# Kernel optimization log

Measured on AMD Instinct MI355X. Metric: run time of the kernel, lower is better.

## Reference

```python
import jax, jax.numpy as jnp
import numpy as np

HEADS = 8
GROUP_SIZE = 256
DIM = 512
QK_DIM = 512
M_GLOBAL = 64


def setup_inputs() -> dict:
    key = jax.random.key(0)
    ks = jax.random.split(key, 9)
    B, N = 2, 16384
    normed_x = jax.random.normal(ks[0], (B, N, DIM), dtype=jnp.float32)
    # idx_last must be a per-batch permutation of [0, N): gather reorders tokens,
    # the final scatter puts them back.
    perm = jnp.stack([jax.random.permutation(jax.random.fold_in(ks[1], b), N) for b in range(B)])
    idx_last = perm[..., None].astype(jnp.int32)  # [B, N, 1]
    dq = QK_DIM // HEADS
    dv = DIM // HEADS
    k_global = jax.random.normal(ks[2], (HEADS, M_GLOBAL, dq), dtype=jnp.float32)
    v_global = jax.random.normal(ks[3], (HEADS, M_GLOBAL, dv), dtype=jnp.float32)
    s = 0.02
    Wq = jax.random.normal(ks[4], (DIM, QK_DIM), dtype=jnp.float32) * s
    Wk = jax.random.normal(ks[5], (DIM, QK_DIM), dtype=jnp.float32) * s
    Wv = jax.random.normal(ks[6], (DIM, DIM), dtype=jnp.float32) * s
    Wproj = jax.random.normal(ks[7], (DIM, DIM), dtype=jnp.float32) * s
    return {"normed_x": normed_x, "idx_last": idx_last, "k_global": k_global,
            "v_global": v_global, "Wq": Wq, "Wk": Wk, "Wv": Wv, "Wproj": Wproj}


def _iasa_forward(normed_x, idx_last, k_global, v_global, Wq, Wk, Wv, Wproj):
    B, N, dim = normed_x.shape
    H = HEADS
    gs = min(N, GROUP_SIZE)
    ng = -(-N // gs)
    pad_n = ng * gs - N
    q = normed_x @ Wq  # [B, N, qk]
    k = normed_x @ Wk  # [B, N, qk]
    v = normed_x @ Wv  # [B, N, dim]
    # gather-reorder tokens
    q = jnp.take_along_axis(q, jnp.broadcast_to(idx_last, q.shape), axis=1)
    k = jnp.take_along_axis(k, jnp.broadcast_to(idx_last, k.shape), axis=1)
    v = jnp.take_along_axis(v, jnp.broadcast_to(idx_last, v.shape), axis=1)
    # pad queries with flipped tail to [B, ng*gs, qk]
    pq = jnp.concatenate([q, q[:, N - pad_n:N][:, ::-1]], axis=1)
    # pad k/v with flipped last (pad_n+gs) tokens -> length (ng+1)*gs
    pk = jnp.concatenate([k, k[:, N - pad_n - gs:N][:, ::-1]], axis=1)
    pv = jnp.concatenate([v, v[:, N - pad_n - gs:N][:, ::-1]], axis=1)
    dq = pq.shape[-1] // H
    dv = dim // H
    # queries: [B, ng, H, gs, dq]
    qg = pq.reshape(B, ng, gs, H, dq).transpose(0, 1, 3, 2, 4)
    # overlapping windows of size 2*gs, stride gs (unfold equivalent)
    kgrp = pk.reshape(B, ng + 1, gs, H, dq)
    vgrp = pv.reshape(B, ng + 1, gs, H, dv)
    kwin = jnp.concatenate([kgrp[:, :-1], kgrp[:, 1:]], axis=2).transpose(0, 1, 3, 2, 4)  # [B,ng,H,2gs,dq]
    vwin = jnp.concatenate([vgrp[:, :-1], vgrp[:, 1:]], axis=2).transpose(0, 1, 3, 2, 4)  # [B,ng,H,2gs,dv]
    scale = 1.0 / jnp.sqrt(jnp.asarray(dq, dtype=qg.dtype))
    # local attention
    s1 = jnp.einsum('bghqd,bghkd->bghqk', qg, kwin) * scale
    out1 = jnp.einsum('bghqk,bghkd->bghqd', jax.nn.softmax(s1, axis=-1), vwin)
    # global attention (k_global/v_global shared across batch and groups)
    s2 = jnp.einsum('bghqd,hmd->bghqm', qg, k_global) * scale
    out2 = jnp.einsum('bghqm,hmd->bghqd', jax.nn.softmax(s2, axis=-1), v_global)
    out = (out1 + out2).transpose(0, 1, 3, 2, 4).reshape(B, ng * gs, H * dv)[:, :N]
    # scatter back (inverse of the gather, since idx_last is a permutation)
    idxo = jnp.broadcast_to(idx_last, out.shape)
    bi = jnp.arange(B)[:, None, None]
    ci = jnp.arange(H * dv)[None, None, :]
    out = out.at[bi, idxo, ci].set(out)
    return out @ Wproj


def reference(normed_x, idx_last, k_global, v_global, Wq, Wk, Wv, Wproj):
    return _iasa_forward(normed_x, idx_last, k_global, v_global, Wq, Wk, Wv, Wproj)
```

## Files before the change

### kernel.cpp

```cpp
#include <hip/hip_runtime.h>
#include <hip/hip_bf16.h>

#define B_   2
#define N_   16384
#define H_   8
#define GS_  256
#define NG_  64

typedef unsigned short u16;
typedef __attribute__((ext_vector_type(8))) short bf16x8;
typedef __attribute__((ext_vector_type(4))) float f32x4;
typedef __attribute__((ext_vector_type(8))) unsigned short us8;
typedef __attribute__((ext_vector_type(4))) unsigned short us4;
typedef __attribute__((ext_vector_type(4))) unsigned int u32x4;

__device__ __forceinline__ u16 f2b(float f){
  union { float f; unsigned u; } v; v.f = f;
  unsigned r = v.u + 0x7fffu + ((v.u >> 16) & 1u);
  return (u16)(r >> 16);
}

__device__ __forceinline__ u16 f2bh(float f){
  __hip_bfloat16 h = __float2bfloat16(f);
  u16 u; __builtin_memcpy(&u, &h, 2);
  return u;
}

__device__ __forceinline__ void gload16(const void* g, const void* lds){
  __builtin_amdgcn_global_load_lds(
      (const __attribute__((address_space(1))) void*)g,
      (__attribute__((address_space(3))) void*)lds, 16, 0, 0);
}

__device__ __forceinline__ bf16x8 lds_read8(const u16* base, int row, int coloff){
  int byte = (row*128 + coloff) ^ ((row & 7) << 4);
  return *(const bf16x8*)((const char*)base + byte);
}

__device__ __forceinline__ void stout(float* p, float v){ *p = v; }
__device__ __forceinline__ void stout(u16* p, float v){ *p = f2b(v); }

__global__ void cvt_f32_bf16(const float4* __restrict__ in, us4* __restrict__ out, int n4){
  int i = blockIdx.x * 256 + threadIdx.x;
  if (i < n4){
    float4 v = in[i];
    us4 o;
    o[0] = f2b(v.x); o[1] = f2b(v.y); o[2] = f2b(v.z); o[3] = f2b(v.w);
    out[i] = o;
  }
}

__global__ void cvt_w_t(const float* __restrict__ W0, const float* __restrict__ W1,
                        const float* __restrict__ W2, const float* __restrict__ W3,
                        u16* __restrict__ T0, u16* __restrict__ T1,
                        u16* __restrict__ T2, u16* __restrict__ T3)
{
  int z = blockIdx.z;
  const float* W = (z==0)?W0:((z==1)?W1:((z==2)?W2:W3));
  u16* T = (z==0)?T0:((z==1)?T1:((z==2)?T2:T3));
  __shared__ float tile[16][17];
  int tx = threadIdx.x & 15, ty = threadIdx.x >> 4;
  int k0 = blockIdx.x*16, n0 = blockIdx.y*16;
  tile[ty][tx] = W[(k0+ty)*512 + n0 + tx];
  __syncthreads();
  T[(n0+ty)*512 + k0 + tx] = f2b(tile[tx][ty]);
}

template<typename OUT_T, bool MULTI, bool GATHA, bool SCATC>
__global__ __launch_bounds__(256, 2) void gemm_bf16k(
    const u16* __restrict__ A,
    const u16* __restrict__ Wt0, const u16* __restrict__ Wt1, const u16* __restrict__ Wt2,
    const int* __restrict__ perm,
    OUT_T* __restrict__ C, int ldc)
{
  __shared__ u16 Al[128*64];
  __shared__ u16 Bl[128*64];
  const int tid = threadIdx.x;
  const int l = tid & 63, w = tid >> 6;
  const int lr = l & 15, lg = l >> 4;
  const int bm = blockIdx.x, bn = blockIdx.y;
  const int wr = (w >> 1) * 64, wc = (w & 1) * 64;

  const u16* Wt; int ocolb; float qsc;
  if (MULTI){
    int wsel = bn >> 2;
    Wt = (wsel == 0) ? Wt0 : ((wsel == 1) ? Wt1 : Wt2);
    ocolb = (bn & 3) * 128;
    qsc = (wsel == 0) ? 0.125f : 1.0f;
  } else { Wt = Wt0; ocolb = bn * 128; qsc = 1.0f; }

  int arows[4];
#pragma unroll
  for (int i = 0; i < 4; ++i){
    int r = bm*128 + i*32 + (tid >> 3);
    arows[i] = GATHA ? ((r & ~(N_-1)) + perm[r]) : r;
  }

  f32x4 acc[4][4];
#pragma unroll
  for (int m = 0; m < 4; ++m)
#pragma unroll
    for (int n = 0; n < 4; ++n) acc[m][n] = (f32x4){0.f,0.f,0.f,0.f};

  const int c8 = tid & 7;
  for (int kk = 0; kk < 512; kk += 64){
#pragma unroll
    for (int i = 0; i < 4; ++i){
      int o = i*4096 + tid*16;
      int brow = o >> 7;
      gload16(A  + (size_t)arows[i]*512 + kk + c8*8, (const char*)Al + i*4096 + w*1024);
      gload16(Wt + (size_t)(ocolb + brow)*512 + kk + c8*8, (const char*)Bl + i*4096 + w*1024);
    }
    __syncthreads();
#pragma unroll
    for (int ks = 0; ks < 2; ++ks){
      bf16x8 af[4], bfv[4];
#pragma unroll
      for (int m = 0; m < 4; ++m) af[m]  = *(const bf16x8*)&Al[(wr + m*16 + lr)*64 + ks*32 + lg*8];
#pragma unroll
      for (int n = 0; n < 4; ++n) bfv[n] = *(const bf16x8*)&Bl[(wc + n*16 + lr)*64 + ks*32 + lg*8];
#pragma unroll
      for (int m = 0; m < 4; ++m)
#pragma unroll
        for (int n = 0; n < 4; ++n)
          acc[m][n] = __builtin_amdgcn_mfma_f32_16x16x32_bf16(af[m], bfv[n], acc[m][n], 0, 0, 0);
    }
    __syncthreads();
  }
#pragma unroll
  for (int m = 0; m < 4; ++m)
#pragma unroll
    for (int n = 0; n < 4; ++n)
#pragma unroll
      for (int j = 0; j < 4; ++j){
        int row = bm*128 + wr + m*16 + lg*4 + j;
        int col = bn*128 + wc + n*16 + lr;
        size_t orow = SCATC ? (size_t)((row & ~(N_-1)) + perm[row]) : (size_t)row;
        stout(&C[orow*ldc + col], acc[m][n][j] * qsc);
      }
}

#define COMPUTE_CHUNK(KBUF, VBUF, ACC, LAC) do { \
  f32x4 s_[4][4]; \
  _Pragma("unroll") \
  for (int m_ = 0; m_ < 4; ++m_){ _Pragma("unroll") for (int n_ = 0; n_ < 4; ++n_) s_[m_][n_] = (f32x4){0.f,0.f,0.f,0.f}; } \
  _Pragma("unroll") \
  for (int ks_ = 0; ks_ < 2; ++ks_){ \
    bf16x8 kf_[4]; \
    _Pragma("unroll") for (int n_ = 0; n_ < 4; ++n_) kf_[n_] = lds_read8((KBUF), n_*16 + lr, ks_*64 + lg*16); \
    _Pragma("unroll") for (int m_ = 0; m_ < 4; ++m_){ \
      _Pragma("unroll") for (int n_ = 0; n_ < 4; ++n_) \
        s_[m_][n_] = __builtin_amdgcn_mfma_f32_16x16x32_bf16(qf[m_][ks_], kf_[n_], s_[m_][n_], 0, 0, 0); } } \
  _Pragma("unroll") \
  for (int m_ = 0; m_ < 4; ++m_){ _Pragma("unroll") for (int j_ = 0; j_ < 4; ++j_){ \
      float rs_ = 0.f; \
      _Pragma("unroll") for (int n_ = 0; n_ < 4; ++n_){ float p_ = __expf(s_[m_][n_][j_]); s_[m_][n_][j_] = p_; rs_ += p_; } \
      (LAC)[m_][j_] += rs_; } } \
  _Pragma("unroll") \
  for (int mh_ = 0; mh_ < 2; ++mh_){ \
    _Pragma("unroll") for (int m2_ = 0; m2_ < 2; ++m2_){ \
      _Pragma("unroll") for (int n_ = 0; n_ < 4; ++n_){ \
        _Pragma("unroll") for (int j_ = 0; j_ < 4; ++j_){ \
          int row_ = m2_*16 + lg*4 + j_, col_ = n_*16 + lr; \
          int byte_ = (row_*128 + col_*2) ^ ((row_ & 7) << 4); \
          *(u16*)((char*)Pw + byte_) = f2bh(s_[mh_*2+m2_][n_][j_]); } } } \
    _Pragma("unroll") for (int ks_ = 0; ks_ < 2; ++ks_){ \
      bf16x8 pa_[2], vb_[4]; \
      _Pragma("unroll") for (int m2_ = 0; m2_ < 2; ++m2_) pa_[m2_] = lds_read8(Pw, m2_*16 + lr, ks_*64 + lg*16); \
      _Pragma("unroll") for (int n_ = 0; n_ < 4; ++n_) vb_[n_] = lds_read8((VBUF), n_*16 + lr, ks_*64 + lg*16); \
      _Pragma("unroll") for (int m2_ = 0; m2_ < 2; ++m2_){ \
        _Pragma("unroll") for (int n_ = 0; n_ < 4; ++n_) \
          (ACC)[mh_*2+m2_][n_] = __builtin_amdgcn_mfma_f32_16x16x32_bf16(pa_[m2_], vb_[n_], (ACC)[mh_*2+m2_][n_], 0, 0, 0); } } \
  } \
} while(0)

#define LOADKV(c) do { int c_ = (c); \
  if (c_ < 8){ \
    int p0k_ = g*GS_ + c_*64 + krow_; \
    int p1k_ = p0k_ + 32; \
    int rk0_ = (p0k_ < N_) ? p0k_ : (2*N_ - 1 - p0k_); \
    int rk1_ = (p1k_ < N_) ? p1k_ : (2*N_ - 1 - p1k_); \
    kr0 = *(const us8*)(qkv + (size_t)(b*N_ + rk0_)*1536 + 512 + h*64 + kc8_*8); \
    kr1 = *(const us8*)(qkv + (size_t)(b*N_ + rk1_)*1536 + 512 + h*64 + kc8_*8); \
    int p0v_ = g*GS_ + c_*64 + 2*pair; \
    int p1v_ = p0v_ + 1; \
    int rv0_ = (p0v_ < N_) ? p0v_ : (2*N_ - 1 - p0v_); \
    int rv1_ = (p1v_ < N_) ? p1v_ : (2*N_ - 1 - p1v_); \
    vr0 = *(const us8*)(qkv + (size_t)(b*N_ + rv0_)*1536 + 1024 + h*64 + dvb*8); \
    vr1 = *(const us8*)(qkv + (size_t)(b*N_ + rv1_)*1536 + 1024 + h*64 + dvb*8); \
  } else { \
    kr0 = *(const us8*)(kgb + (size_t)(h*64 + krow_)*64 + kc8_*8); \
    kr1 = *(const us8*)(kgb + (size_t)(h*64 + 32 + krow_)*64 + kc8_*8); \
    vr0 = *(const us8*)(vgb + (size_t)(h*64 + 2*pair)*64 + dvb*8); \
    vr1 = *(const us8*)(vgb + (size_t)(h*64 + 2*pair + 1)*64 + dvb*8); \
  } } while(0)

#define WRITEKV() do { \
  { int r0_ = krow_, r1_ = 32 + krow_; \
    *(us8*)((char*)Kb + ((r0_*128 + kc8_*16) ^ ((r0_ & 7) << 4))) = kr0; \
    *(us8*)((char*)Kb + ((r1_*128 + kc8_*16) ^ ((r1_ & 7) << 4))) = kr1; } \
  _Pragma("unroll") \
  for (int j_ = 0; j_ < 8; ++j_){ \
    int r_ = dvb*8 + j_; \
    int byte_ = (r_*128 + pair*4) ^ ((r_ & 7) << 4); \
    *(unsigned*)((char*)Vb + byte_) = (unsigned)vr0[j_] | ((unsigned)vr1[j_] << 16); } \
} while(0)

__global__ __launch_bounds__(256, 2) void attn_kernel(
    const u16* __restrict__ qkv,
    const u16* __restrict__ kgb,
    const u16* __restrict__ vgb,
    u16* __restrict__ outp)
{
  __shared__ u16 Pl[4][32*64];
  __shared__ u16 Kb[64*64];
  __shared__ u16 Vb[64*64];

  const int tid = threadIdx.x;
  const int l = tid & 63, w = tid >> 6;
  const int lr = l & 15, lg = l >> 4;
  const int pair = tid & 31, dvb = tid >> 5;
  const int krow_ = tid >> 3, kc8_ = tid & 7;

  const int g = blockIdx.x, h = blockIdx.y, b = blockIdx.z;

  bf16x8 qf[4][2];
#pragma unroll
  for (int m = 0; m < 4; ++m){
    int grow = g*GS_ + w*64 + m*16 + lr;
    const u16* qrow = qkv + (size_t)(b*N_ + grow)*1536 + h*64;
#pragma unroll
    for (int ks = 0; ks < 2; ++ks)
      qf[m][ks] = *(const bf16x8*)(qrow + ks*32 + lg*8);
  }

  u16* Pw = Pl[w];

  us8 kr0, kr1, vr0, vr1;
  LOADKV(0);
  WRITEKV();
  __syncthreads();

  f32x4 oacc[4][4];
  float lrun[4][4];
#pragma unroll
  for (int m = 0; m < 4; ++m)
#pragma unroll
    for (int n = 0; n < 4; ++n) oacc[m][n] = (f32x4){0.f,0.f,0.f,0.f};
#pragma unroll
  for (int m = 0; m < 4; ++m)
#pragma unroll
    for (int j = 0; j < 4; ++j) lrun[m][j] = 0.f;

  for (int c = 0; c < 8; ++c){
    LOADKV(c + 1);
    COMPUTE_CHUNK(Kb, Vb, oacc, lrun);
    __syncthreads();
    WRITEKV();
    __syncthreads();
  }

#pragma unroll
  for (int m = 0; m < 4; ++m)
#pragma unroll
    for (int j = 0; j < 4; ++j){
      float s1 = lrun[m][j];
      s1 += __shfl_xor(s1, 1); s1 += __shfl_xor(s1, 2);
      s1 += __shfl_xor(s1, 4); s1 += __shfl_xor(s1, 8);
      float i1 = 1.f / s1;
#pragma unroll
      for (int n = 0; n < 4; ++n) oacc[m][n][j] *= i1;
    }

  {
    f32x4 s_[4][4];
#pragma unroll
    for (int m_ = 0; m_ < 4; ++m_)
#pragma unroll
      for (int n_ = 0; n_ < 4; ++n_) s_[m_][n_] = (f32x4){0.f,0.f,0.f,0.f};
#pragma unroll
    for (int ks_ = 0; ks_ < 2; ++ks_){
      bf16x8 kf_[4];
#pragma unroll
      for (int n_ = 0; n_ < 4; ++n_) kf_[n_] = lds_read8(Kb, n_*16 + lr, ks_*64 + lg*16);
#pragma unroll
      for (int m_ = 0; m_ < 4; ++m_)
#pragma unroll
        for (int n_ = 0; n_ < 4; ++n_)
          s_[m_][n_] = __builtin_amdgcn_mfma_f32_16x16x32_bf16(qf[m_][ks_], kf_[n_], s_[m_][n_], 0, 0, 0);
    }
#pragma unroll
    for (int m_ = 0; m_ < 4; ++m_)
#pragma unroll
      for (int j_ = 0; j_ < 4; ++j_){
        float rs_ = 0.f;
#pragma unroll
        for (int n_ = 0; n_ < 4; ++n_){ float p_ = __expf(s_[m_][n_][j_]); s_[m_][n_][j_] = p_; rs_ += p_; }
        rs_ += __shfl_xor(rs_, 1); rs_ += __shfl_xor(rs_, 2);
        rs_ += __shfl_xor(rs_, 4); rs_ += __shfl_xor(rs_, 8);
        float iv_ = 1.f / rs_;
#pragma unroll
        for (int n_ = 0; n_ < 4; ++n_) s_[m_][n_][j_] *= iv_;
      }
#pragma unroll
    for (int mh_ = 0; mh_ < 2; ++mh_){
#pragma unroll
      for (int m2_ = 0; m2_ < 2; ++m2_){
#pragma unroll
        for (int n_ = 0; n_ < 4; ++n_){
#pragma unroll
          for (int j_ = 0; j_ < 4; ++j_){
            int row_ = m2_*16 + lg*4 + j_, col_ = n_*16 + lr;
            int byte_ = (row_*128 + col_*2) ^ ((row_ & 7) << 4);
            *(u16*)((char*)Pw + byte_) = f2bh(s_[mh_*2+m2_][n_][j_]);
          }
        }
      }
#pragma unroll
      for (int ks_ = 0; ks_ < 2; ++ks_){
        bf16x8 pa_[2], vb_[4];
#pragma unroll
        for (int m2_ = 0; m2_ < 2; ++m2_) pa_[m2_] = lds_read8(Pw, m2_*16 + lr, ks_*64 + lg*16);
#pragma unroll
        for (int n_ = 0; n_ < 4; ++n_) vb_[n_] = lds_read8(Vb, n_*16 + lr, ks_*64 + lg*16);
#pragma unroll
        for (int m2_ = 0; m2_ < 2; ++m2_)
#pragma unroll
          for (int n_ = 0; n_ < 4; ++n_)
            oacc[mh_*2+m2_][n_] = __builtin_amdgcn_mfma_f32_16x16x32_bf16(pa_[m2_], vb_[n_], oacc[mh_*2+m2_][n_], 0, 0, 0);
      }
    }
  }

#pragma unroll
  for (int mh = 0; mh < 2; ++mh){
#pragma unroll
    for (int m2 = 0; m2 < 2; ++m2)
#pragma unroll
      for (int n = 0; n < 4; ++n)
#pragma unroll
        for (int j = 0; j < 4; ++j){
          int row = m2*16 + lg*4 + j, col = n*16 + lr;
          int byte = (row*128 + col*2) ^ ((row & 7) << 4);
          *(u16*)((char*)Pw + byte) = f2bh(oacc[mh*2+m2][n][j]);
        }
    __builtin_amdgcn_s_waitcnt(0);
#pragma unroll
    for (int i4 = 0; i4 < 4; ++i4){
      int o = i4*1024 + l*16;
      int row = o >> 7, c8 = (o & 127) >> 4;
      int addr = o ^ ((row & 7) << 4);
      u32x4 d = *(const u32x4*)((const char*)Pw + addr);
      int orow = g*GS_ + w*64 + mh*32 + row;
      *(u32x4*)(outp + (size_t)(b*N_ + orow)*512 + h*64 + c8*8) = d;
    }
  }
}

extern "C" void kernel_launch(void* const* d_in, const int* in_sizes, int n_in,
                              void* d_out, int out_size, void* d_ws, size_t ws_size,
                              hipStream_t stream)
{
  const float* x  = (const float*)d_in[0];
  const int*  idx = (const int*)d_in[1];
  const float* kg = (const float*)d_in[2];
  const float* vg = (const float*)d_in[3];
  const float* Wq = (const float*)d_in[4];
  const float* Wk = (const float*)d_in[5];
  const float* Wv = (const float*)d_in[6];
  const float* Wp = (const float*)d_in[7];
  float* out = (float*)d_out;

  char* ws = (char*)d_ws;
  u16* Xb   = (u16*)ws;
  u16* qkv  = (u16*)(ws + 33554432);
  u16* Wqt  = (u16*)(ws + 134217728);
  u16* Wkt  = (u16*)(ws + 134217728 + 524288);
  u16* Wvt  = (u16*)(ws + 134217728 + 2*524288);
  u16* Wpt  = (u16*)(ws + 134217728 + 3*524288);
  u16* kgb  = (u16*)(ws + 134217728 + 4*524288);
  u16* vgb  = (u16*)(ws + 134217728 + 4*524288 + 65536);
  u16* attn_o = Xb;

  cvt_f32_bf16<<<16384, 256, 0, stream>>>((const float4*)x, (us4*)Xb, 16777216/4);
  cvt_f32_bf16<<<32, 256, 0, stream>>>((const float4*)kg, (us4*)kgb, 32768/4);
  cvt_f32_bf16<<<32, 256, 0, stream>>>((const float4*)vg, (us4*)vgb, 32768/4);
  cvt_w_t<<<dim3(32,32,4), 256, 0, stream>>>(Wq, Wk, Wv, Wp, Wqt, Wkt, Wvt, Wpt);
  gemm_bf16k<u16, true, true, false><<<dim3(256,12), 256, 0, stream>>>(Xb, Wqt, Wkt, Wvt, idx, qkv, 1536);
  attn_kernel<<<dim3(64,8,2), 256, 0, stream>>>(qkv, kgb, vgb, attn_o);
  gemm_bf16k<float, false, false, true><<<dim3(256,4), 256, 0, stream>>>(attn_o, Wpt, Wpt, Wpt, idx, out, 512);
}
```

Before: 220.5 us.

## Split attention blocks to 128 queries and use exp2 with log2e-folded scale

```diff
diff --git a/kernel.cpp b/kernel.cpp
--- a/kernel.cpp
+++ b/kernel.cpp
@@ -86,7 +86,7 @@
     int wsel = bn >> 2;
     Wt = (wsel == 0) ? Wt0 : ((wsel == 1) ? Wt1 : Wt2);
     ocolb = (bn & 3) * 128;
-    qsc = (wsel == 0) ? 0.125f : 1.0f;
+    qsc = (wsel == 0) ? 0.18033688f : 1.0f;
   } else { Wt = Wt0; ocolb = bn * 128; qsc = 1.0f; }
 
   int arows[4];
@@ -141,37 +141,35 @@
 }
 
 #define COMPUTE_CHUNK(KBUF, VBUF, ACC, LAC) do { \
-  f32x4 s_[4][4]; \
-  _Pragma("unroll") \
-  for (int m_ = 0; m_ < 4; ++m_){ _Pragma("unroll") for (int n_ = 0; n_ < 4; ++n_) s_[m_][n_] = (f32x4){0.f,0.f,0.f,0.f}; } \
+  f32x4 s_[2][4]; \
+  _Pragma("unroll") \
+  for (int m_ = 0; m_ < 2; ++m_){ _Pragma("unroll") for (int n_ = 0; n_ < 4; ++n_) s_[m_][n_] = (f32x4){0.f,0.f,0.f,0.f}; } \
   _Pragma("unroll") \
   for (int ks_ = 0; ks_ < 2; ++ks_){ \
     bf16x8 kf_[4]; \
     _Pragma("unroll") for (int n_ = 0; n_ < 4; ++n_) kf_[n_] = lds_read8((KBUF), n_*16 + lr, ks_*64 + lg*16); \
-    _Pragma("unroll") for (int m_ = 0; m_ < 4; ++m_){ \
+    _Pragma("unroll") for (int m_ = 0; m_ < 2; ++m_){ \
       _Pragma("unroll") for (int n_ = 0; n_ < 4; ++n_) \
         s_[m_][n_] = __builtin_amdgcn_mfma_f32_16x16x32_bf16(qf[m_][ks_], kf_[n_], s_[m_][n_], 0, 0, 0); } } \
   _Pragma("unroll") \
-  for (int m_ = 0; m_ < 4; ++m_){ _Pragma("unroll") for (int j_ = 0; j_ < 4; ++j_){ \
+  for (int m_ = 0; m_ < 2; ++m_){ _Pragma("unroll") for (int j_ = 0; j_ < 4; ++j_){ \
       float rs_ = 0.f; \
-      _Pragma("unroll") for (int n_ = 0; n_ < 4; ++n_){ float p_ = __expf(s_[m_][n_][j_]); s_[m_][n_][j_] = p_; rs_ += p_; } \
+      _Pragma("unroll") for (int n_ = 0; n_ < 4; ++n_){ float p_ = exp2f(s_[m_][n_][j_]); s_[m_][n_][j_] = p_; rs_ += p_; } \
       (LAC)[m_][j_] += rs_; } } \
   _Pragma("unroll") \
-  for (int mh_ = 0; mh_ < 2; ++mh_){ \
-    _Pragma("unroll") for (int m2_ = 0; m2_ < 2; ++m2_){ \
-      _Pragma("unroll") for (int n_ = 0; n_ < 4; ++n_){ \
-        _Pragma("unroll") for (int j_ = 0; j_ < 4; ++j_){ \
-          int row_ = m2_*16 + lg*4 + j_, col_ = n_*16 + lr; \
-          int byte_ = (row_*128 + col_*2) ^ ((row_ & 7) << 4); \
-          *(u16*)((char*)Pw + byte_) = f2bh(s_[mh_*2+m2_][n_][j_]); } } } \
-    _Pragma("unroll") for (int ks_ = 0; ks_ < 2; ++ks_){ \
-      bf16x8 pa_[2], vb_[4]; \
-      _Pragma("unroll") for (int m2_ = 0; m2_ < 2; ++m2_) pa_[m2_] = lds_read8(Pw, m2_*16 + lr, ks_*64 + lg*16); \
-      _Pragma("unroll") for (int n_ = 0; n_ < 4; ++n_) vb_[n_] = lds_read8((VBUF), n_*16 + lr, ks_*64 + lg*16); \
-      _Pragma("unroll") for (int m2_ = 0; m2_ < 2; ++m2_){ \
-        _Pragma("unroll") for (int n_ = 0; n_ < 4; ++n_) \
-          (ACC)[mh_*2+m2_][n_] = __builtin_amdgcn_mfma_f32_16x16x32_bf16(pa_[m2_], vb_[n_], (ACC)[mh_*2+m2_][n_], 0, 0, 0); } } \
-  } \
+  for (int m_ = 0; m_ < 2; ++m_){ _Pragma("unroll") for (int n_ = 0; n_ < 4; ++n_){ \
+      _Pragma("unroll") for (int j_ = 0; j_ < 4; ++j_){ \
+        int row_ = m_*16 + lg*4 + j_, col_ = n_*16 + lr; \
+        int byte_ = (row_*128 + col_*2) ^ ((row_ & 7) << 4); \
+        *(u16*)((char*)Pw + byte_) = f2bh(s_[m_][n_][j_]); } } } \
+  _Pragma("unroll") \
+  for (int ks_ = 0; ks_ < 2; ++ks_){ \
+    bf16x8 pa_[2], vb_[4]; \
+    _Pragma("unroll") for (int m_ = 0; m_ < 2; ++m_) pa_[m_] = lds_read8(Pw, m_*16 + lr, ks_*64 + lg*16); \
+    _Pragma("unroll") for (int n_ = 0; n_ < 4; ++n_) vb_[n_] = lds_read8((VBUF), n_*16 + lr, ks_*64 + lg*16); \
+    _Pragma("unroll") for (int m_ = 0; m_ < 2; ++m_){ \
+      _Pragma("unroll") for (int n_ = 0; n_ < 4; ++n_) \
+        (ACC)[m_][n_] = __builtin_amdgcn_mfma_f32_16x16x32_bf16(pa_[m_], vb_[n_], (ACC)[m_][n_], 0, 0, 0); } } \
 } while(0)
 
 #define LOADKV(c) do { int c_ = (c); \
@@ -222,12 +220,14 @@
   const int pair = tid & 31, dvb = tid >> 5;
   const int krow_ = tid >> 3, kc8_ = tid & 7;
 
-  const int g = blockIdx.x, h = blockIdx.y, b = blockIdx.z;
-
-  bf16x8 qf[4][2];
-#pragma unroll
-  for (int m = 0; m < 4; ++m){
-    int grow = g*GS_ + w*64 + m*16 + lr;
+  const int g2 = blockIdx.x, h = blockIdx.y, b = blockIdx.z;
+  const int g = g2 >> 1;
+  const int qbase = g2*128 + w*32;
+
+  bf16x8 qf[2][2];
+#pragma unroll
+  for (int m = 0; m < 2; ++m){
+    int grow = qbase + m*16 + lr;
     const u16* qrow = qkv + (size_t)(b*N_ + grow)*1536 + h*64;
 #pragma unroll
     for (int ks = 0; ks < 2; ++ks)
@@ -241,14 +241,14 @@
   WRITEKV();
   __syncthreads();
 
-  f32x4 oacc[4][4];
-  float lrun[4][4];
-#pragma unroll
-  for (int m = 0; m < 4; ++m)
+  f32x4 oacc[2][4];
+  float lrun[2][4];
+#pragma unroll
+  for (int m = 0; m < 2; ++m)
 #pragma unroll
     for (int n = 0; n < 4; ++n) oacc[m][n] = (f32x4){0.f,0.f,0.f,0.f};
 #pragma unroll
-  for (int m = 0; m < 4; ++m)
+  for (int m = 0; m < 2; ++m)
 #pragma unroll
     for (int j = 0; j < 4; ++j) lrun[m][j] = 0.f;
 
@@ -261,7 +261,7 @@
   }
 
 #pragma unroll
-  for (int m = 0; m < 4; ++m)
+  for (int m = 0; m < 2; ++m)
 #pragma unroll
     for (int j = 0; j < 4; ++j){
       float s1 = lrun[m][j];
@@ -273,9 +273,9 @@
     }
 
   {
-    f32x4 s_[4][4];
-#pragma unroll
-    for (int m_ = 0; m_ < 4; ++m_)
+    f32x4 s_[2][4];
+#pragma unroll
+    for (int m_ = 0; m_ < 2; ++m_)
 #pragma unroll
       for (int n_ = 0; n_ < 4; ++n_) s_[m_][n_] = (f32x4){0.f,0.f,0.f,0.f};
 #pragma unroll
@@ -284,18 +284,18 @@
 #pragma unroll
       for (int n_ = 0; n_ < 4; ++n_) kf_[n_] = lds_read8(Kb, n_*16 + lr, ks_*64 + lg*16);
 #pragma unroll
-      for (int m_ = 0; m_ < 4; ++m_)
+      for (int m_ = 0; m_ < 2; ++m_)
 #pragma unroll
         for (int n_ = 0; n_ < 4; ++n_)
           s_[m_][n_] = __builtin_amdgcn_mfma_f32_16x16x32_bf16(qf[m_][ks_], kf_[n_], s_[m_][n_], 0, 0, 0);
     }
 #pragma unroll
-    for (int m_ = 0; m_ < 4; ++m_)
+    for (int m_ = 0; m_ < 2; ++m_)
 #pragma unroll
       for (int j_ = 0; j_ < 4; ++j_){
         float rs_ = 0.f;
 #pragma unroll
-        for (int n_ = 0; n_ < 4; ++n_){ float p_ = __expf(s_[m_][n_][j_]); s_[m_][n_][j_] = p_; rs_ += p_; }
+        for (int n_ = 0; n_ < 4; ++n_){ float p_ = exp2f(s_[m_][n_][j_]); s_[m_][n_][j_] = p_; rs_ += p_; }
         rs_ += __shfl_xor(rs_, 1); rs_ += __shfl_xor(rs_, 2);
         rs_ += __shfl_xor(rs_, 4); rs_ += __shfl_xor(rs_, 8);
         float iv_ = 1.f / rs_;
@@ -303,57 +303,49 @@
         for (int n_ = 0; n_ < 4; ++n_) s_[m_][n_][j_] *= iv_;
       }
 #pragma unroll
-    for (int mh_ = 0; mh_ < 2; ++mh_){
-#pragma unroll
-      for (int m2_ = 0; m2_ < 2; ++m2_){
-#pragma unroll
-        for (int n_ = 0; n_ < 4; ++n_){
-#pragma unroll
-          for (int j_ = 0; j_ < 4; ++j_){
-            int row_ = m2_*16 + lg*4 + j_, col_ = n_*16 + lr;
-            int byte_ = (row_*128 + col_*2) ^ ((row_ & 7) << 4);
-            *(u16*)((char*)Pw + byte_) = f2bh(s_[mh_*2+m2_][n_][j_]);
-          }
+    for (int m_ = 0; m_ < 2; ++m_)
+#pragma unroll
+      for (int n_ = 0; n_ < 4; ++n_)
+#pragma unroll
+        for (int j_ = 0; j_ < 4; ++j_){
+          int row_ = m_*16 + lg*4 + j_, col_ = n_*16 + lr;
+          int byte_ = (row_*128 + col_*2) ^ ((row_ & 7) << 4);
+          *(u16*)((char*)Pw + byte_) = f2bh(s_[m_][n_][j_]);
         }
+#pragma unroll
+    for (int ks_ = 0; ks_ < 2; ++ks_){
+      bf16x8 pa_[2], vb_[4];
+#pragma unroll
+      for (int m_ = 0; m_ < 2; ++m_) pa_[m_] = lds_read8(Pw, m_*16 + lr, ks_*64 + lg*16);
+#pragma unroll
+      for (int n_ = 0; n_ < 4; ++n_) vb_[n_] = lds_read8(Vb, n_*16 + lr, ks_*64 + lg*16);
+#pragma unroll
+      for (int m_ = 0; m_ < 2; ++m_)
+#pragma unroll
+        for (int n_ = 0; n_ < 4; ++n_)
+          oacc[m_][n_] = __builtin_amdgcn_mfma_f32_16x16x32_bf16(pa_[m_], vb_[n_], oacc[m_][n_], 0, 0, 0);
+    }
+  }
+
+#pragma unroll
+  for (int m = 0; m < 2; ++m)
+#pragma unroll
+    for (int n = 0; n < 4; ++n)
+#pragma unroll
+      for (int j = 0; j < 4; ++j){
+        int row = m*16 + lg*4 + j, col = n*16 + lr;
+        int byte = (row*128 + col*2) ^ ((row & 7) << 4);
+        *(u16*)((char*)Pw + byte) = f2bh(oacc[m][n][j]);
       }
-#pragma unroll
-      for (int ks_ = 0; ks_ < 2; ++ks_){
-        bf16x8 pa_[2], vb_[4];
-#pragma unroll
-        for (int m2_ = 0; m2_ < 2; ++m2_) pa_[m2_] = lds_read8(Pw, m2_*16 + lr, ks_*64 + lg*16);
-#pragma unroll
-        for (int n_ = 0; n_ < 4; ++n_) vb_[n_] = lds_read8(Vb, n_*16 + lr, ks_*64 + lg*16);
-#pragma unroll
-        for (int m2_ = 0; m2_ < 2; ++m2_)
-#pragma unroll
-          for (int n_ = 0; n_ < 4; ++n_)
-            oacc[mh_*2+m2_][n_] = __builtin_amdgcn_mfma_f32_16x16x32_bf16(pa_[m2_], vb_[n_], oacc[mh_*2+m2_][n_], 0, 0, 0);
-      }
-    }
-  }
-
-#pragma unroll
-  for (int mh = 0; mh < 2; ++mh){
-#pragma unroll
-    for (int m2 = 0; m2 < 2; ++m2)
-#pragma unroll
-      for (int n = 0; n < 4; ++n)
-#pragma unroll
-        for (int j = 0; j < 4; ++j){
-          int row = m2*16 + lg*4 + j, col = n*16 + lr;
-          int byte = (row*128 + col*2) ^ ((row & 7) << 4);
-          *(u16*)((char*)Pw + byte) = f2bh(oacc[mh*2+m2][n][j]);
-        }
-    __builtin_amdgcn_s_waitcnt(0);
-#pragma unroll
-    for (int i4 = 0; i4 < 4; ++i4){
-      int o = i4*1024 + l*16;
-      int row = o >> 7, c8 = (o & 127) >> 4;
-      int addr = o ^ ((row & 7) << 4);
-      u32x4 d = *(const u32x4*)((const char*)Pw + addr);
-      int orow = g*GS_ + w*64 + mh*32 + row;
-      *(u32x4*)(outp + (size_t)(b*N_ + orow)*512 + h*64 + c8*8) = d;
-    }
+  __builtin_amdgcn_s_waitcnt(0);
+#pragma unroll
+  for (int i4 = 0; i4 < 4; ++i4){
+    int o = i4*1024 + l*16;
+    int row = o >> 7, c8 = (o & 127) >> 4;
+    int addr = o ^ ((row & 7) << 4);
+    u32x4 d = *(const u32x4*)((const char*)Pw + addr);
+    int orow = qbase + row;
+    *(u32x4*)(outp + (size_t)(b*N_ + orow)*512 + h*64 + c8*8) = d;
   }
 }
 
@@ -387,6 +379,6 @@
   cvt_f32_bf16<<<32, 256, 0, stream>>>((const float4*)vg, (us4*)vgb, 32768/4);
   cvt_w_t<<<dim3(32,32,4), 256, 0, stream>>>(Wq, Wk, Wv, Wp, Wqt, Wkt, Wvt, Wpt);
   gemm_bf16k<u16, true, true, false><<<dim3(256,12), 256, 0, stream>>>(Xb, Wqt, Wkt, Wvt, idx, qkv, 1536);
-  attn_kernel<<<dim3(64,8,2), 256, 0, stream>>>(qkv, kgb, vgb, attn_o);
+  attn_kernel<<<dim3(128,8,2), 256, 0, stream>>>(qkv, kgb, vgb, attn_o);
   gemm_bf16k<float, false, false, true><<<dim3(256,4), 256, 0, stream>>>(attn_o, Wpt, Wpt, Wpt, idx, out, 512);
 }
```

After: 225.2 us. +2.1%, slower.

## Compute transposed scores so P tiles pack into vector LDS stores, use exp2

Applied to the files above, without the earlier changes.

```diff
diff --git a/kernel.cpp b/kernel.cpp
--- a/kernel.cpp
+++ b/kernel.cpp
@@ -13,6 +13,7 @@
 typedef __attribute__((ext_vector_type(8))) unsigned short us8;
 typedef __attribute__((ext_vector_type(4))) unsigned short us4;
 typedef __attribute__((ext_vector_type(4))) unsigned int u32x4;
+typedef __attribute__((ext_vector_type(2))) unsigned int u32x2;
 
 __device__ __forceinline__ u16 f2b(float f){
   union { float f; unsigned u; } v; v.f = f;
@@ -24,6 +25,10 @@
   __hip_bfloat16 h = __float2bfloat16(f);
   u16 u; __builtin_memcpy(&u, &h, 2);
   return u;
+}
+
+__device__ __forceinline__ unsigned pk2(float a, float b){
+  return ((unsigned)f2b(b) << 16) | (unsigned)f2b(a);
 }
 
 __device__ __forceinline__ void gload16(const void* g, const void* lds){
@@ -86,7 +91,7 @@
     int wsel = bn >> 2;
     Wt = (wsel == 0) ? Wt0 : ((wsel == 1) ? Wt1 : Wt2);
     ocolb = (bn & 3) * 128;
-    qsc = (wsel == 0) ? 0.125f : 1.0f;
+    qsc = (wsel == 0) ? 0.18033688f : 1.0f;
   } else { Wt = Wt0; ocolb = bn * 128; qsc = 1.0f; }
 
   int arows[4];
@@ -143,27 +148,32 @@
 #define COMPUTE_CHUNK(KBUF, VBUF, ACC, LAC) do { \
   f32x4 s_[4][4]; \
   _Pragma("unroll") \
-  for (int m_ = 0; m_ < 4; ++m_){ _Pragma("unroll") for (int n_ = 0; n_ < 4; ++n_) s_[m_][n_] = (f32x4){0.f,0.f,0.f,0.f}; } \
+  for (int n_ = 0; n_ < 4; ++n_){ _Pragma("unroll") for (int m_ = 0; m_ < 4; ++m_) s_[n_][m_] = (f32x4){0.f,0.f,0.f,0.f}; } \
   _Pragma("unroll") \
   for (int ks_ = 0; ks_ < 2; ++ks_){ \
     bf16x8 kf_[4]; \
     _Pragma("unroll") for (int n_ = 0; n_ < 4; ++n_) kf_[n_] = lds_read8((KBUF), n_*16 + lr, ks_*64 + lg*16); \
-    _Pragma("unroll") for (int m_ = 0; m_ < 4; ++m_){ \
-      _Pragma("unroll") for (int n_ = 0; n_ < 4; ++n_) \
-        s_[m_][n_] = __builtin_amdgcn_mfma_f32_16x16x32_bf16(qf[m_][ks_], kf_[n_], s_[m_][n_], 0, 0, 0); } } \
+    _Pragma("unroll") for (int n_ = 0; n_ < 4; ++n_){ \
+      _Pragma("unroll") for (int m_ = 0; m_ < 4; ++m_) \
+        s_[n_][m_] = __builtin_amdgcn_mfma_f32_16x16x32_bf16(kf_[n_], qf[m_][ks_], s_[n_][m_], 0, 0, 0); } } \
   _Pragma("unroll") \
-  for (int m_ = 0; m_ < 4; ++m_){ _Pragma("unroll") for (int j_ = 0; j_ < 4; ++j_){ \
-      float rs_ = 0.f; \
-      _Pragma("unroll") for (int n_ = 0; n_ < 4; ++n_){ float p_ = __expf(s_[m_][n_][j_]); s_[m_][n_][j_] = p_; rs_ += p_; } \
-      (LAC)[m_][j_] += rs_; } } \
+  for (int m_ = 0; m_ < 4; ++m_){ \
+    float rs_ = 0.f; \
+    _Pragma("unroll") for (int n_ = 0; n_ < 4; ++n_){ \
+      _Pragma("unroll") for (int j_ = 0; j_ < 4; ++j_){ \
+        float p_ = exp2f(s_[n_][m_][j_]); s_[n_][m_][j_] = p_; rs_ += p_; } } \
+    (LAC)[m_] += rs_; } \
   _Pragma("unroll") \
   for (int mh_ = 0; mh_ < 2; ++mh_){ \
     _Pragma("unroll") for (int m2_ = 0; m2_ < 2; ++m2_){ \
+      int m_ = mh_*2 + m2_; \
+      int q_ = m2_*16 + lr; \
       _Pragma("unroll") for (int n_ = 0; n_ < 4; ++n_){ \
-        _Pragma("unroll") for (int j_ = 0; j_ < 4; ++j_){ \
-          int row_ = m2_*16 + lg*4 + j_, col_ = n_*16 + lr; \
-          int byte_ = (row_*128 + col_*2) ^ ((row_ & 7) << 4); \
-          *(u16*)((char*)Pw + byte_) = f2bh(s_[mh_*2+m2_][n_][j_]); } } } \
+        u32x2 pk_; \
+        pk_[0] = pk2(s_[n_][m_][0], s_[n_][m_][1]); \
+        pk_[1] = pk2(s_[n_][m_][2], s_[n_][m_][3]); \
+        int byte_ = (q_*128 + n_*32 + lg*8) ^ ((q_ & 7) << 4); \
+        *(u32x2*)((char*)Pw + byte_) = pk_; } } \
     _Pragma("unroll") for (int ks_ = 0; ks_ < 2; ++ks_){ \
       bf16x8 pa_[2], vb_[4]; \
       _Pragma("unroll") for (int m2_ = 0; m2_ < 2; ++m2_) pa_[m2_] = lds_read8(Pw, m2_*16 + lr, ks_*64 + lg*16); \
@@ -242,15 +252,13 @@
   __syncthreads();
 
   f32x4 oacc[4][4];
-  float lrun[4][4];
+  float lrun[4];
 #pragma unroll
   for (int m = 0; m < 4; ++m)
 #pragma unroll
     for (int n = 0; n < 4; ++n) oacc[m][n] = (f32x4){0.f,0.f,0.f,0.f};
 #pragma unroll
-  for (int m = 0; m < 4; ++m)
-#pragma unroll
-    for (int j = 0; j < 4; ++j) lrun[m][j] = 0.f;
+  for (int m = 0; m < 4; ++m) lrun[m] = 0.f;
 
   for (int c = 0; c < 8; ++c){
     LOADKV(c + 1);
@@ -260,60 +268,68 @@
     __syncthreads();
   }
 
+  float i1[4];
+#pragma unroll
+  for (int m = 0; m < 4; ++m){
+    float s1 = lrun[m];
+    s1 += __shfl_xor(s1, 16); s1 += __shfl_xor(s1, 32);
+    i1[m] = 1.f / s1;
+  }
 #pragma unroll
   for (int m = 0; m < 4; ++m)
 #pragma unroll
     for (int j = 0; j < 4; ++j){
-      float s1 = lrun[m][j];
-      s1 += __shfl_xor(s1, 1); s1 += __shfl_xor(s1, 2);
-      s1 += __shfl_xor(s1, 4); s1 += __shfl_xor(s1, 8);
-      float i1 = 1.f / s1;
-#pragma unroll
-      for (int n = 0; n < 4; ++n) oacc[m][n][j] *= i1;
+      float invb = __shfl(i1[m], lg*4 + j);
+#pragma unroll
+      for (int n = 0; n < 4; ++n) oacc[m][n][j] *= invb;
     }
 
   {
     f32x4 s_[4][4];
 #pragma unroll
-    for (int m_ = 0; m_ < 4; ++m_)
-#pragma unroll
-      for (int n_ = 0; n_ < 4; ++n_) s_[m_][n_] = (f32x4){0.f,0.f,0.f,0.f};
+    for (int n_ = 0; n_ < 4; ++n_)
+#pragma unroll
+      for (int m_ = 0; m_ < 4; ++m_) s_[n_][m_] = (f32x4){0.f,0.f,0.f,0.f};
 #pragma unroll
     for (int ks_ = 0; ks_ < 2; ++ks_){
       bf16x8 kf_[4];
 #pragma unroll
       for (int n_ = 0; n_ < 4; ++n_) kf_[n_] = lds_read8(Kb, n_*16 + lr, ks_*64 + lg*16);
 #pragma unroll
-      for (int m_ = 0; m_ < 4; ++m_)
-#pragma unroll
-        for (int n_ = 0; n_ < 4; ++n_)
-          s_[m_][n_] = __builtin_amdgcn_mfma_f32_16x16x32_bf16(qf[m_][ks_], kf_[n_], s_[m_][n_], 0, 0, 0);
-    }
-#pragma unroll
-    for (int m_ = 0; m_ < 4; ++m_)
-#pragma unroll
-      for (int j_ = 0; j_ < 4; ++j_){
-        float rs_ = 0.f;
-#pragma unroll
-        for (int n_ = 0; n_ < 4; ++n_){ float p_ = __expf(s_[m_][n_][j_]); s_[m_][n_][j_] = p_; rs_ += p_; }
-        rs_ += __shfl_xor(rs_, 1); rs_ += __shfl_xor(rs_, 2);
-        rs_ += __shfl_xor(rs_, 4); rs_ += __shfl_xor(rs_, 8);
-        float iv_ = 1.f / rs_;
-#pragma unroll
-        for (int n_ = 0; n_ < 4; ++n_) s_[m_][n_][j_] *= iv_;
-      }
+      for (int n_ = 0; n_ < 4; ++n_)
+#pragma unroll
+        for (int m_ = 0; m_ < 4; ++m_)
+          s_[n_][m_] = __builtin_amdgcn_mfma_f32_16x16x32_bf16(kf_[n_], qf[m_][ks_], s_[n_][m_], 0, 0, 0);
+    }
+#pragma unroll
+    for (int m_ = 0; m_ < 4; ++m_){
+      float rs_ = 0.f;
+#pragma unroll
+      for (int n_ = 0; n_ < 4; ++n_)
+#pragma unroll
+        for (int j_ = 0; j_ < 4; ++j_){
+          float p_ = exp2f(s_[n_][m_][j_]); s_[n_][m_][j_] = p_; rs_ += p_;
+        }
+      rs_ += __shfl_xor(rs_, 16); rs_ += __shfl_xor(rs_, 32);
+      float iv_ = 1.f / rs_;
+#pragma unroll
+      for (int n_ = 0; n_ < 4; ++n_)
+#pragma unroll
+        for (int j_ = 0; j_ < 4; ++j_) s_[n_][m_][j_] *= iv_;
+    }
 #pragma unroll
     for (int mh_ = 0; mh_ < 2; ++mh_){
 #pragma unroll
       for (int m2_ = 0; m2_ < 2; ++m2_){
+        int m_ = mh_*2 + m2_;
+        int q_ = m2_*16 + lr;
 #pragma unroll
         for (int n_ = 0; n_ < 4; ++n_){
-#pragma unroll
-          for (int j_ = 0; j_ < 4; ++j_){
-            int row_ = m2_*16 + lg*4 + j_, col_ = n_*16 + lr;
-            int byte_ = (row_*128 + col_*2) ^ ((row_ & 7) << 4);
-            *(u16*)((char*)Pw + byte_) = f2bh(s_[mh_*2+m2_][n_][j_]);
-          }
+          u32x2 pk_;
+          pk_[0] = pk2(s_[n_][m_][0], s_[n_][m_][1]);
+          pk_[1] = pk2(s_[n_][m_][2], s_[n_][m_][3]);
+          int byte_ = (q_*128 + n_*32 + lg*8) ^ ((q_ & 7) << 4);
+          *(u32x2*)((char*)Pw + byte_) = pk_;
         }
       }
 #pragma unroll
```

Result: faster. 213.8 us (-3.0%).
